# Performance work log

Hardware: AMD Instinct MI355X
Metric: run time of the kernel (lower is better)

## Reference

```python
import jax, jax.numpy as jnp
import numpy as np

B, L, D, H, NLAYERS = 32, 2048, 1024, 16, 4
HD = D // H
NEG = -1e30


def setup_inputs() -> dict:
    key = jax.random.key(0)
    ks = jax.random.split(key, 12)
    tokens = jax.random.normal(ks[0], (B, L, D), dtype=jnp.float32)
    lengths = jax.random.randint(ks[1], (B,), 1, L + 1, dtype=jnp.int32)
    query_token = jax.random.normal(ks[2], (1, D), dtype=jnp.float32)
    s = 0.02
    Wq = jax.random.normal(ks[3], (NLAYERS, D, D), dtype=jnp.float32) * s
    Wk = jax.random.normal(ks[4], (NLAYERS, D, D), dtype=jnp.float32) * s
    Wv = jax.random.normal(ks[5], (NLAYERS, D, D), dtype=jnp.float32) * s
    Wo = jax.random.normal(ks[6], (NLAYERS, D, D), dtype=jnp.float32) * s
    bq = jnp.zeros((NLAYERS, D), jnp.float32)
    bk = jnp.zeros((NLAYERS, D), jnp.float32)
    bv = jnp.zeros((NLAYERS, D), jnp.float32)
    bo = jnp.zeros((NLAYERS, D), jnp.float32)
    gamma = jnp.ones((NLAYERS, D), jnp.float32)
    beta = jnp.zeros((NLAYERS, D), jnp.float32)
    return dict(tokens=tokens, lengths=lengths, query_token=query_token,
                Wq=Wq, bq=bq, Wk=Wk, bk=bk, Wv=Wv, bv=bv, Wo=Wo, bo=bo,
                gamma=gamma, beta=beta)


def _layernorm(x, g, b):
    mu = jnp.mean(x, axis=-1, keepdims=True)
    var = jnp.mean(jnp.square(x - mu), axis=-1, keepdims=True)
    return (x - mu) * jax.lax.rsqrt(var + 1e-5) * g + b


def reference(tokens, lengths, query_token, Wq, bq, Wk, bk, Wv, bv, Wo, bo, gamma, beta):
    # valid[b, l] = True where token l exists (inverse of key_padding_mask)
    valid = jnp.arange(L)[None, :] < lengths[:, None]            # [B, L]
    scale = 1.0 / jnp.sqrt(jnp.float32(HD))
    # zero out padded positions like the torch padded buffer (math-neutral)
    toks = tokens * valid[:, :, None].astype(tokens.dtype)       # [B, L, D]
    q = jnp.broadcast_to(query_token[None], (B, 1, D))           # [B, 1, D]
    for i in range(NLAYERS):
        qh = (q @ Wq[i] + bq[i]).reshape(B, 1, H, HD)            # [B, 1, H, hd]
        kh = (toks @ Wk[i] + bk[i]).reshape(B, L, H, HD)         # [B, L, H, hd]
        vh = (toks @ Wv[i] + bv[i]).reshape(B, L, H, HD)
        scores = jnp.einsum('bqhd,bkhd->bhqk', qh, kh) * scale   # [B, H, 1, L]
        scores = jnp.where(valid[:, None, None, :], scores, NEG)
        attn = jax.nn.softmax(scores, axis=-1)
        out = jnp.einsum('bhqk,bkhd->bqhd', attn, vh).reshape(B, 1, D)
        out = out @ Wo[i] + bo[i]
        q = _layernorm(out, gamma[i], beta[i])
    return q[:, 0, :]                                            # [B, D]
```

## Files before the change

kernel.cpp:

```cpp
#include <hip/hip_runtime.h>
#include <hip/hip_bf16.h>
#include <cstdint>
#include <cstddef>

#define BB 32
#define LL 2048
#define DD 1024
#define HH 16
#define HDIM 64
#define NL 4
#define NCHUNK 8
#define CHUNK 256
#define NEGINF -1e30f

typedef __attribute__((ext_vector_type(8))) short bf16x8;
typedef __attribute__((ext_vector_type(4))) float f32x4;

__device__ __forceinline__ unsigned short f2b(float x) {
    union { float f; unsigned int u; } v; v.f = x;
    unsigned int r = (v.u + 0x7FFFu + ((v.u >> 16) & 1u)) >> 16;
    return (unsigned short)r;
}

template<int SRC, int KSP>
__global__ __launch_bounds__(256) void k_gemv(
        const float* __restrict__ Xg,
        const float* __restrict__ stats, const float* __restrict__ gamma,
        const float* __restrict__ beta,
        const float* __restrict__ parts_in, const float* __restrict__ bias_in,
        const float* __restrict__ ctx_p, const float* __restrict__ m_p,
        const float* __restrict__ s_p,
        const float* __restrict__ W, float* __restrict__ outp) {
    constexpr int KL = DD / KSP;
    int bid = blockIdx.x, tid = threadIdx.x;
    int ct = bid & 15, ks = bid >> 4;
    int e0 = ks * KL;
    __shared__ float Xs[BB][KL];
    __shared__ float wgtS[BB][NCHUNK];
    __shared__ float mgS[BB], SgS[BB];
    if (SRC == 3) {
        if (tid < BB) {
            int b = tid; float m = NEGINF;
            for (int c8 = 0; c8 < NCHUNK; ++c8)
                m = fmaxf(m, m_p[(b * NCHUNK + c8) * HH + ct]);
            float S = 0.f;
            for (int c8 = 0; c8 < NCHUNK; ++c8)
                S += s_p[(b * NCHUNK + c8) * HH + ct] *
                     __expf(m_p[(b * NCHUNK + c8) * HH + ct] - m);
            mgS[b] = m; SgS[b] = S;
        }
        __syncthreads();
        {
            int b = tid >> 3, c8 = tid & 7;
            wgtS[b][c8] = __expf(m_p[(b * NCHUNK + c8) * HH + ct] - mgS[b]) / SgS[b];
        }
        __syncthreads();
    }
    for (int j = 0; j < (BB * KL) / 256; ++j) {
        int i = tid + j * 256;
        int b = i / KL, k = i % KL;
        float x;
        if (SRC == 0) {
            x = Xg[e0 + k];
        } else if (SRC == 1) {
            float mu = stats[b * 2], rstd = stats[b * 2 + 1];
            x = (Xg[(size_t)b * DD + e0 + k] - mu) * rstd * gamma[e0 + k] + beta[e0 + k];
        } else if (SRC == 2) {
            x = bias_in[e0 + k];
#pragma unroll
            for (int j2 = 0; j2 < 32; ++j2)
                x += parts_in[((size_t)(j2 * BB) + b) * DD + e0 + k];
        } else {
            x = 0.f;
#pragma unroll
            for (int c8 = 0; c8 < NCHUNK; ++c8)
                x += wgtS[b][c8] *
                     ctx_p[(((size_t)(b * NCHUNK + c8)) * HH + ct) * DD + e0 + k];
        }
        Xs[b][k] = x;
    }
    __syncthreads();
    int col = tid & 63, bg = tid >> 6;
    int c = ct * 64 + col;
    float acc[8] = {0.f, 0.f, 0.f, 0.f, 0.f, 0.f, 0.f, 0.f};
    for (int k = 0; k < KL; k += 4) {
        float w0 = W[(size_t)(e0 + k) * DD + c];
        float w1 = W[(size_t)(e0 + k + 1) * DD + c];
        float w2 = W[(size_t)(e0 + k + 2) * DD + c];
        float w3 = W[(size_t)(e0 + k + 3) * DD + c];
#pragma unroll
        for (int bb = 0; bb < 8; ++bb) {
            const float4 xv = *(const float4*)&Xs[bg * 8 + bb][k];
            acc[bb] += xv.x * w0 + xv.y * w1 + xv.z * w2 + xv.w * w3;
        }
    }
#pragma unroll
    for (int bb = 0; bb < 8; ++bb)
        outp[((size_t)(ks * BB) + bg * 8 + bb) * DD + c] = acc[bb];
}

__global__ __launch_bounds__(1024) void k_stats(const float* __restrict__ parts,
        const float* __restrict__ bo, float* __restrict__ oraw,
        float* __restrict__ stats) {
    int b = blockIdx.x, c = threadIdx.x;
    float v = bo[c];
#pragma unroll
    for (int ks = 0; ks < 8; ++ks)
        v += parts[((size_t)(ks * BB) + b) * DD + c];
    oraw[(size_t)b * DD + c] = v;
    float s1 = v, s2 = v * v;
#pragma unroll
    for (int off = 32; off; off >>= 1) {
        s1 += __shfl_xor(s1, off);
        s2 += __shfl_xor(s2, off);
    }
    __shared__ float r1[16], r2[16];
    int w = c >> 6;
    if ((c & 63) == 0) { r1[w] = s1; r2[w] = s2; }
    __syncthreads();
    if (c == 0) {
        float a = 0.f, q = 0.f;
#pragma unroll
        for (int i = 0; i < 16; ++i) { a += r1[i]; q += r2[i]; }
        float mu = a / (float)DD, var = q / (float)DD - mu * mu;
        stats[b * 2] = mu;
        stats[b * 2 + 1] = rsqrtf(var + 1e-5f);
    }
}

__global__ __launch_bounds__(256) void k_final(const float* __restrict__ oraw,
        const float* __restrict__ stats, const float* __restrict__ gamma,
        const float* __restrict__ beta, float* __restrict__ outp) {
    int i = blockIdx.x * 256 + threadIdx.x;
    int b = i >> 10, c = i & (DD - 1);
    outp[i] = (oraw[i] - stats[b * 2]) * stats[b * 2 + 1] * gamma[c] + beta[c];
}

__global__ __launch_bounds__(256) void k_wk(const float* __restrict__ qp,
        const float* __restrict__ bq,
        const float* __restrict__ Wk, const float* __restrict__ bk,
        unsigned short* __restrict__ wk16, float* __restrict__ sb) {
    int h = blockIdx.x >> 4, et = blockIdx.x & 15;
    int tid = threadIdx.x;
    __shared__ float qs[BB][HDIM + 1];
    for (int i = tid; i < BB * HDIM; i += 256) {
        int bb = i >> 6, d = i & 63;
        float v = bq[h * HDIM + d];
#pragma unroll
        for (int ks = 0; ks < 8; ++ks)
            v += qp[((size_t)(ks * BB + bb)) * DD + h * HDIM + d];
        qs[bb][d] = v;
    }
    __syncthreads();
    int b = tid & 31, eo = tid >> 5;
    for (int k = 0; k < 8; ++k) {
        int e = et * 64 + eo * 8 + k;
        const float* wrow = Wk + (size_t)e * DD + h * HDIM;
        float acc = 0.f;
#pragma unroll
        for (int d = 0; d < HDIM; ++d) acc += qs[b][d] * wrow[d];
        wk16[((size_t)(b * HH + h)) * DD + e] = f2b(acc);
    }
    if (et == 0 && tid < BB) {
        float acc = 0.f;
#pragma unroll
        for (int d = 0; d < HDIM; ++d) acc += qs[tid][d] * bk[h * HDIM + d];
        sb[tid * HH + h] = acc;
    }
}

template<int MODE>
__global__ __launch_bounds__(1024) void k_attn(const float* __restrict__ toks,
        unsigned short* __restrict__ tcache,
        const int* __restrict__ lens, const unsigned short* __restrict__ wk16,
        const float* __restrict__ sb, float* __restrict__ ctx_p,
        float* __restrict__ m_p, float* __restrict__ s_p) {
    int b = blockIdx.x >> 3, chunk = blockIdx.x & 7;
    int tid = threadIdx.x, lane = tid & 63, w = tid >> 6;
    int len = lens[b];
    int base = chunk * CHUNK;
    int pidx = (b * NCHUNK + chunk) * HH;
    if (base >= len) {
        if (tid < HH) { m_p[pidx + tid] = NEGINF; s_p[pidx + tid] = 0.f; }
        return;
    }
    int nv = min(CHUNK, len - base);
    int ng = (nv + 31) >> 5;

    __shared__ __align__(16) unsigned short Tr[32][1032];
    __shared__ float Sred[16][HH][34];
    __shared__ unsigned short Pt[HH][40];
    __shared__ float sm_m[HH], sm_s[HH], sm_c[HH];

    if (tid < HH) { sm_m[tid] = NEGINF; sm_s[tid] = 0.f; }

    int hq = lane & 15, qg = lane >> 4;
    const unsigned short* wkb = wk16 + ((size_t)(b * HH + hq)) * DD + w * 64 + 8 * qg;
    bf16x8 afr0 = *(const bf16x8*)(wkb);
    bf16x8 afr1 = *(const bf16x8*)(wkb + 32);
    f32x4 zer = {0.f, 0.f, 0.f, 0.f};
    f32x4 ctxacc[4] = {zer, zer, zer, zer};
    float sbh = (tid < 512) ? sb[b * HH + (tid >> 5)] : 0.f;
    int st = tid >> 7;
    int se = (tid & 127) * 8;
    const size_t rowbase = (size_t)(b * LL + base);

    bf16x8 pc[4];
    float4 pa[4], pb[4];
    auto LOADG = [&](int g) {
        if (MODE == 2) {
            const unsigned short* s0p = tcache + (rowbase + g * 32) * DD + se;
#pragma unroll
            for (int p = 0; p < 4; ++p)
                pc[p] = *(const bf16x8*)(s0p + (size_t)(p * 8 + st) * DD);
        } else {
            const float* s0p = toks + (rowbase + g * 32) * DD + se;
#pragma unroll
            for (int p = 0; p < 4; ++p) {
                const float* sp = s0p + (size_t)(p * 8 + st) * DD;
                pa[p] = *(const float4*)sp;
                pb[p] = *(const float4*)(sp + 4);
            }
        }
    };
    LOADG(0);
    __syncthreads();

    for (int g = 0; g < ng; ++g) {
        int t0 = g * 32;
        if (MODE == 2) {
#pragma unroll
            for (int p = 0; p < 4; ++p)
                *(bf16x8*)&Tr[p * 8 + st][se] = pc[p];
        } else {
#pragma unroll
            for (int p = 0; p < 4; ++p) {
                bf16x8 v;
                v[0] = f2b(pa[p].x); v[1] = f2b(pa[p].y);
                v[2] = f2b(pa[p].z); v[3] = f2b(pa[p].w);
                v[4] = f2b(pb[p].x); v[5] = f2b(pb[p].y);
                v[6] = f2b(pb[p].z); v[7] = f2b(pb[p].w);
                *(bf16x8*)&Tr[p * 8 + st][se] = v;
                if (MODE == 1)
                    *(bf16x8*)(tcache + (rowbase + t0 + p * 8 + st) * DD + se) = v;
            }
        }
        if (g + 1 < ng) LOADG(g + 1);
        __syncthreads();
        f32x4 s0 = zer, s1 = zer;
        {
            int eb = w * 64 + 8 * qg;
            s0 = __builtin_amdgcn_mfma_f32_16x16x32_bf16(afr0, *(const bf16x8*)&Tr[hq][eb], s0, 0, 0, 0);
            s0 = __builtin_amdgcn_mfma_f32_16x16x32_bf16(afr1, *(const bf16x8*)&Tr[hq][eb + 32], s0, 0, 0, 0);
            s1 = __builtin_amdgcn_mfma_f32_16x16x32_bf16(afr0, *(const bf16x8*)&Tr[16 + hq][eb], s1, 0, 0, 0);
            s1 = __builtin_amdgcn_mfma_f32_16x16x32_bf16(afr1, *(const bf16x8*)&Tr[16 + hq][eb + 32], s1, 0, 0, 0);
        }
#pragma unroll
        for (int r = 0; r < 4; ++r) {
            Sred[w][qg * 4 + r][hq] = s0[r];
            Sred[w][qg * 4 + r][16 + hq] = s1[r];
        }
        __syncthreads();
        if (tid < 512) {
            int h = tid >> 5, t = tid & 31;
            float s = 0.f;
#pragma unroll
            for (int ww = 0; ww < 16; ++ww) s += Sred[ww][h][t];
            s = (s + sbh) * 0.125f;
            bool valid = (t0 + t) < nv;
            if (!valid) s = NEGINF;
            float tm = s;
#pragma unroll
            for (int off = 16; off; off >>= 1) tm = fmaxf(tm, __shfl_xor(tm, off, 32));
            float oldm = sm_m[h];
            float newm = fmaxf(oldm, tm);
            float pv = valid ? __expf(s - newm) : 0.f;
            float ps = pv;
#pragma unroll
            for (int off = 16; off; off >>= 1) ps += __shfl_xor(ps, off, 32);
            if (t == 0) {
                float corr = __expf(oldm - newm);
                sm_c[h] = corr;
                sm_m[h] = newm;
                sm_s[h] = sm_s[h] * corr + ps;
            }
            Pt[h][t] = f2b(pv);
        }
        __syncthreads();
        {
            float cr[4];
#pragma unroll
            for (int r = 0; r < 4; ++r) cr[r] = sm_c[qg * 4 + r];
            bf16x8 pafr;
            ushort4 pa0 = *(const ushort4*)&Pt[hq][8 * qg];
            ushort4 pa1 = *(const ushort4*)&Pt[hq][8 * qg + 4];
            pafr[0] = pa0.x; pafr[1] = pa0.y; pafr[2] = pa0.z; pafr[3] = pa0.w;
            pafr[4] = pa1.x; pafr[5] = pa1.y; pafr[6] = pa1.z; pafr[7] = pa1.w;
#pragma unroll
            for (int et = 0; et < 4; ++et) {
#pragma unroll
                for (int r = 0; r < 4; ++r) ctxacc[et][r] *= cr[r];
                bf16x8 bfr;
                int ec = w * 64 + et * 16 + hq;
#pragma unroll
                for (int i = 0; i < 8; ++i) bfr[i] = (short)Tr[8 * qg + i][ec];
                ctxacc[et] = __builtin_amdgcn_mfma_f32_16x16x32_bf16(pafr, bfr, ctxacc[et], 0, 0, 0);
            }
        }
        __syncthreads();
    }
    if (tid < HH) { m_p[pidx + tid] = sm_m[tid]; s_p[pidx + tid] = sm_s[tid]; }
#pragma unroll
    for (int et = 0; et < 4; ++et)
#pragma unroll
        for (int r = 0; r < 4; ++r) {
            int h = qg * 4 + r, e = w * 64 + et * 16 + hq;
            ctx_p[((size_t)pidx + h) * DD + e] = ctxacc[et][r];
        }
}

extern "C" void kernel_launch(void* const* d_in, const int* in_sizes, int n_in,
                              void* d_out, int out_size, void* d_ws, size_t ws_size,
                              hipStream_t stream) {
    const float* toks  = (const float*)d_in[0];
    const int*   lens  = (const int*)d_in[1];
    const float* qt    = (const float*)d_in[2];
    const float* Wq    = (const float*)d_in[3];
    const float* bq    = (const float*)d_in[4];
    const float* Wk    = (const float*)d_in[5];
    const float* bk    = (const float*)d_in[6];
    const float* Wv    = (const float*)d_in[7];
    const float* bv    = (const float*)d_in[8];
    const float* Wo    = (const float*)d_in[9];
    const float* bo    = (const float*)d_in[10];
    const float* gamma = (const float*)d_in[11];
    const float* beta  = (const float*)d_in[12];
    float* out = (float*)d_out;
    float* ws  = (float*)d_ws;

    float* ctx_p = ws;
    float* m_p   = ws + 4194304;
    float* s_p   = ws + 4198400;
    float* pvp   = ws + 4202496;
    float* op    = ws + 5251072;
    float* qp    = ws + 5513216;
    float* oraw  = ws + 5775360;
    float* stats = ws + 5808128;
    float* sbuf  = ws + 5808192;
    unsigned short* wk16 = (unsigned short*)(ws + 5808704);
    const size_t base_floats = 6070848;
    unsigned short* tcache = (unsigned short*)(ws + base_floats);
    const size_t need_cache = base_floats * 4 + (size_t)BB * LL * DD * 2;
    const bool use_cache = (ws_size >= need_cache);

    k_gemv<0, 8><<<128, 256, 0, stream>>>(qt, nullptr, nullptr, nullptr,
            nullptr, nullptr, nullptr, nullptr, nullptr, Wq, qp);
    k_wk<<<256, 256, 0, stream>>>(qp, bq, Wk, bk, wk16, sbuf);

    for (int i = 0; i < NL; ++i) {
        if (use_cache) {
            if (i == 0)
                k_attn<1><<<256, 1024, 0, stream>>>(toks, tcache, lens, wk16,
                        sbuf, ctx_p, m_p, s_p);
            else
                k_attn<2><<<256, 1024, 0, stream>>>(toks, tcache, lens, wk16,
                        sbuf, ctx_p, m_p, s_p);
        } else {
            k_attn<0><<<256, 1024, 0, stream>>>(toks, tcache, lens, wk16,
                    sbuf, ctx_p, m_p, s_p);
        }
        const float* Wv_i = Wv + (size_t)i * DD * DD;
        const float* Wo_i = Wo + (size_t)i * DD * DD;
        k_gemv<3, 32><<<512, 256, 0, stream>>>(nullptr, nullptr, nullptr, nullptr,
                nullptr, nullptr, ctx_p, m_p, s_p, Wv_i, pvp);
        k_gemv<2, 8><<<128, 256, 0, stream>>>(nullptr, nullptr, nullptr, nullptr,
                pvp, bv + i * DD, nullptr, nullptr, nullptr, Wo_i, op);
        k_stats<<<32, 1024, 0, stream>>>(op, bo + i * DD, oraw, stats);
        if (i == NL - 1) {
            k_final<<<128, 256, 0, stream>>>(oraw, stats, gamma + i * DD,
                    beta + i * DD, out);
        } else {
            k_gemv<1, 8><<<128, 256, 0, stream>>>(oraw, stats, gamma + i * DD,
                    beta + i * DD, nullptr, nullptr, nullptr, nullptr, nullptr,
                    Wq + (size_t)(i + 1) * DD * DD, qp);
            k_wk<<<256, 256, 0, stream>>>(qp, bq + (i + 1) * DD,
                    Wk + (size_t)(i + 1) * DD * DD, bk + (i + 1) * DD,
                    wk16, sbuf);
        }
    }
}
```

Before: 402.6 us.

## Store attention partials in bf16, unify GEMV split, fuse final layernorm, drop prefetch

Attention partial context outputs are now written as bf16 instead of fp32, which halves the traffic between the attention kernel and the Wv GEMV. All GEMVs now use a uniform 16-way K split with 256 blocks, and the downstream reductions are adjusted to match. The final layernorm is folded into the stats kernel, removing one launch. The register prefetch of the next token group in the attention kernel is removed in favour of a simpler load-then-compute loop. The bf16 partials add rounding error, and losing the prefetch may expose load latency.

```diff
diff --git a/kernel.cpp b/kernel.cpp
--- a/kernel.cpp
+++ b/kernel.cpp
@@ -12,6 +12,7 @@
 #define NCHUNK 8
 #define CHUNK 256
 #define NEGINF -1e30f
+#define PKS 16
 
 typedef __attribute__((ext_vector_type(8))) short bf16x8;
 typedef __attribute__((ext_vector_type(4))) float f32x4;
@@ -21,17 +22,21 @@
     unsigned int r = (v.u + 0x7FFFu + ((v.u >> 16) & 1u)) >> 16;
     return (unsigned short)r;
 }
-
-template<int SRC, int KSP>
+__device__ __forceinline__ float b2f(unsigned short u) {
+    union { unsigned int u; float f; } v; v.u = ((unsigned int)u) << 16;
+    return v.f;
+}
+
+template<int SRC>
 __global__ __launch_bounds__(256) void k_gemv(
         const float* __restrict__ Xg,
         const float* __restrict__ stats, const float* __restrict__ gamma,
         const float* __restrict__ beta,
         const float* __restrict__ parts_in, const float* __restrict__ bias_in,
-        const float* __restrict__ ctx_p, const float* __restrict__ m_p,
+        const unsigned short* __restrict__ ctx16, const float* __restrict__ m_p,
         const float* __restrict__ s_p,
         const float* __restrict__ W, float* __restrict__ outp) {
-    constexpr int KL = DD / KSP;
+    constexpr int KL = DD / PKS;
     int bid = blockIdx.x, tid = threadIdx.x;
     int ct = bid & 15, ks = bid >> 4;
     int e0 = ks * KL;
@@ -56,9 +61,10 @@
         }
         __syncthreads();
     }
-    for (int j = 0; j < (BB * KL) / 256; ++j) {
+#pragma unroll
+    for (int j = 0; j < 8; ++j) {
         int i = tid + j * 256;
-        int b = i / KL, k = i % KL;
+        int b = i >> 6, k = i & 63;
         float x;
         if (SRC == 0) {
             x = Xg[e0 + k];
@@ -68,14 +74,14 @@
         } else if (SRC == 2) {
             x = bias_in[e0 + k];
 #pragma unroll
-            for (int j2 = 0; j2 < 32; ++j2)
+            for (int j2 = 0; j2 < PKS; ++j2)
                 x += parts_in[((size_t)(j2 * BB) + b) * DD + e0 + k];
         } else {
             x = 0.f;
 #pragma unroll
             for (int c8 = 0; c8 < NCHUNK; ++c8)
                 x += wgtS[b][c8] *
-                     ctx_p[(((size_t)(b * NCHUNK + c8)) * HH + ct) * DD + e0 + k];
+                     b2f(ctx16[(((size_t)(b * NCHUNK + c8)) * HH + ct) * DD + e0 + k]);
         }
         Xs[b][k] = x;
     }
@@ -99,15 +105,17 @@
         outp[((size_t)(ks * BB) + bg * 8 + bb) * DD + c] = acc[bb];
 }
 
+template<int LAST>
 __global__ __launch_bounds__(1024) void k_stats(const float* __restrict__ parts,
-        const float* __restrict__ bo, float* __restrict__ oraw,
-        float* __restrict__ stats) {
+        const float* __restrict__ bo, const float* __restrict__ gamma,
+        const float* __restrict__ beta, float* __restrict__ oraw,
+        float* __restrict__ stats, float* __restrict__ outp) {
     int b = blockIdx.x, c = threadIdx.x;
     float v = bo[c];
 #pragma unroll
-    for (int ks = 0; ks < 8; ++ks)
+    for (int ks = 0; ks < PKS; ++ks)
         v += parts[((size_t)(ks * BB) + b) * DD + c];
-    oraw[(size_t)b * DD + c] = v;
+    if (!LAST) oraw[(size_t)b * DD + c] = v;
     float s1 = v, s2 = v * v;
 #pragma unroll
     for (int off = 32; off; off >>= 1) {
@@ -115,6 +123,7 @@
         s2 += __shfl_xor(s2, off);
     }
     __shared__ float r1[16], r2[16];
+    __shared__ float smu, srs;
     int w = c >> 6;
     if ((c & 63) == 0) { r1[w] = s1; r2[w] = s2; }
     __syncthreads();
@@ -123,17 +132,14 @@
 #pragma unroll
         for (int i = 0; i < 16; ++i) { a += r1[i]; q += r2[i]; }
         float mu = a / (float)DD, var = q / (float)DD - mu * mu;
+        float rs = rsqrtf(var + 1e-5f);
+        smu = mu; srs = rs;
         stats[b * 2] = mu;
-        stats[b * 2 + 1] = rsqrtf(var + 1e-5f);
-    }
-}
-
-__global__ __launch_bounds__(256) void k_final(const float* __restrict__ oraw,
-        const float* __restrict__ stats, const float* __restrict__ gamma,
-        const float* __restrict__ beta, float* __restrict__ outp) {
-    int i = blockIdx.x * 256 + threadIdx.x;
-    int b = i >> 10, c = i & (DD - 1);
-    outp[i] = (oraw[i] - stats[b * 2]) * stats[b * 2 + 1] * gamma[c] + beta[c];
+        stats[b * 2 + 1] = rs;
+    }
+    __syncthreads();
+    if (LAST)
+        outp[(size_t)b * DD + c] = (v - smu) * srs * gamma[c] + beta[c];
 }
 
 __global__ __launch_bounds__(256) void k_wk(const float* __restrict__ qp,
@@ -147,7 +153,7 @@
         int bb = i >> 6, d = i & 63;
         float v = bq[h * HDIM + d];
 #pragma unroll
-        for (int ks = 0; ks < 8; ++ks)
+        for (int ks = 0; ks < PKS; ++ks)
             v += qp[((size_t)(ks * BB + bb)) * DD + h * HDIM + d];
         qs[bb][d] = v;
     }
@@ -173,7 +179,7 @@
 __global__ __launch_bounds__(1024) void k_attn(const float* __restrict__ toks,
         unsigned short* __restrict__ tcache,
         const int* __restrict__ lens, const unsigned short* __restrict__ wk16,
-        const float* __restrict__ sb, float* __restrict__ ctx_p,
+        const float* __restrict__ sb, unsigned short* __restrict__ ctx16,
         float* __restrict__ m_p, float* __restrict__ s_p) {
     int b = blockIdx.x >> 3, chunk = blockIdx.x & 7;
     int tid = threadIdx.x, lane = tid & 63, w = tid >> 6;
@@ -185,7 +191,6 @@
         return;
     }
     int nv = min(CHUNK, len - base);
-    int ng = (nv + 31) >> 5;
 
     __shared__ __align__(16) unsigned short Tr[32][1032];
     __shared__ float Sred[16][HH][34];
@@ -203,49 +208,35 @@
     float sbh = (tid < 512) ? sb[b * HH + (tid >> 5)] : 0.f;
     int st = tid >> 7;
     int se = (tid & 127) * 8;
-    const size_t rowbase = (size_t)(b * LL + base);
-
-    bf16x8 pc[4];
-    float4 pa[4], pb[4];
-    auto LOADG = [&](int g) {
+    __syncthreads();
+
+    for (int g = 0; g < 8; ++g) {
+        int t0 = g * 32;
+        if (t0 >= nv) break;
         if (MODE == 2) {
-            const unsigned short* s0p = tcache + (rowbase + g * 32) * DD + se;
-#pragma unroll
-            for (int p = 0; p < 4; ++p)
-                pc[p] = *(const bf16x8*)(s0p + (size_t)(p * 8 + st) * DD);
+            const unsigned short* srcr = tcache + ((size_t)(b * LL + base + t0)) * DD;
+#pragma unroll
+            for (int p = 0; p < 4; ++p) {
+                int t = p * 8 + st;
+                bf16x8 v = *(const bf16x8*)(srcr + (size_t)t * DD + se);
+                *(bf16x8*)&Tr[t][se] = v;
+            }
         } else {
-            const float* s0p = toks + (rowbase + g * 32) * DD + se;
+            const float* srcr = toks + ((size_t)(b * LL + base + t0)) * DD;
 #pragma unroll
             for (int p = 0; p < 4; ++p) {
-                const float* sp = s0p + (size_t)(p * 8 + st) * DD;
-                pa[p] = *(const float4*)sp;
-                pb[p] = *(const float4*)(sp + 4);
+                int t = p * 8 + st;
+                const float* sp = srcr + (size_t)t * DD + se;
+                float4 a0 = *(const float4*)sp;
+                float4 a1 = *(const float4*)(sp + 4);
+                bf16x8 v;
+                v[0] = f2b(a0.x); v[1] = f2b(a0.y); v[2] = f2b(a0.z); v[3] = f2b(a0.w);
+                v[4] = f2b(a1.x); v[5] = f2b(a1.y); v[6] = f2b(a1.z); v[7] = f2b(a1.w);
+                *(bf16x8*)&Tr[t][se] = v;
+                if (MODE == 1)
+                    *(bf16x8*)(tcache + ((size_t)(b * LL + base + t0 + t)) * DD + se) = v;
             }
         }
-    };
-    LOADG(0);
-    __syncthreads();
-
-    for (int g = 0; g < ng; ++g) {
-        int t0 = g * 32;
-        if (MODE == 2) {
-#pragma unroll
-            for (int p = 0; p < 4; ++p)
-                *(bf16x8*)&Tr[p * 8 + st][se] = pc[p];
-        } else {
-#pragma unroll
-            for (int p = 0; p < 4; ++p) {
-                bf16x8 v;
-                v[0] = f2b(pa[p].x); v[1] = f2b(pa[p].y);
-                v[2] = f2b(pa[p].z); v[3] = f2b(pa[p].w);
-                v[4] = f2b(pb[p].x); v[5] = f2b(pb[p].y);
-                v[6] = f2b(pb[p].z); v[7] = f2b(pb[p].w);
-                *(bf16x8*)&Tr[p * 8 + st][se] = v;
-                if (MODE == 1)
-                    *(bf16x8*)(tcache + (rowbase + t0 + p * 8 + st) * DD + se) = v;
-            }
-        }
-        if (g + 1 < ng) LOADG(g + 1);
         __syncthreads();
         f32x4 s0 = zer, s1 = zer;
         {
@@ -315,7 +306,7 @@
 #pragma unroll
         for (int r = 0; r < 4; ++r) {
             int h = qg * 4 + r, e = w * 64 + et * 16 + hq;
-            ctx_p[((size_t)pidx + h) * DD + e] = ctxacc[et][r];
+            ctx16[((size_t)pidx + h) * DD + e] = f2b(ctxacc[et][r]);
         }
 }
 
@@ -338,22 +329,22 @@
     float* out = (float*)d_out;
     float* ws  = (float*)d_ws;
 
-    float* ctx_p = ws;
-    float* m_p   = ws + 4194304;
-    float* s_p   = ws + 4198400;
-    float* pvp   = ws + 4202496;
-    float* op    = ws + 5251072;
-    float* qp    = ws + 5513216;
-    float* oraw  = ws + 5775360;
-    float* stats = ws + 5808128;
-    float* sbuf  = ws + 5808192;
-    unsigned short* wk16 = (unsigned short*)(ws + 5808704);
-    const size_t base_floats = 6070848;
+    unsigned short* ctx16 = (unsigned short*)ws;
+    float* m_p   = ws + 2097152;
+    float* s_p   = ws + 2101248;
+    float* pvp   = ws + 2105344;
+    float* op    = ws + 2629632;
+    float* qp    = ws + 3153920;
+    float* oraw  = ws + 3678208;
+    float* stats = ws + 3710976;
+    float* sbuf  = ws + 3711040;
+    unsigned short* wk16 = (unsigned short*)(ws + 3711552);
+    const size_t base_floats = 3973696;
     unsigned short* tcache = (unsigned short*)(ws + base_floats);
     const size_t need_cache = base_floats * 4 + (size_t)BB * LL * DD * 2;
     const bool use_cache = (ws_size >= need_cache);
 
-    k_gemv<0, 8><<<128, 256, 0, stream>>>(qt, nullptr, nullptr, nullptr,
+    k_gemv<0><<<256, 256, 0, stream>>>(qt, nullptr, nullptr, nullptr,
             nullptr, nullptr, nullptr, nullptr, nullptr, Wq, qp);
     k_wk<<<256, 256, 0, stream>>>(qp, bq, Wk, bk, wk16, sbuf);
 
@@ -361,26 +352,27 @@
         if (use_cache) {
             if (i == 0)
                 k_attn<1><<<256, 1024, 0, stream>>>(toks, tcache, lens, wk16,
-                        sbuf, ctx_p, m_p, s_p);
+                        sbuf, ctx16, m_p, s_p);
             else
                 k_attn<2><<<256, 1024, 0, stream>>>(toks, tcache, lens, wk16,
-                        sbuf, ctx_p, m_p, s_p);
+                        sbuf, ctx16, m_p, s_p);
         } else {
             k_attn<0><<<256, 1024, 0, stream>>>(toks, tcache, lens, wk16,
-                    sbuf, ctx_p, m_p, s_p);
+                    sbuf, ctx16, m_p, s_p);
         }
         const float* Wv_i = Wv + (size_t)i * DD * DD;
         const float* Wo_i = Wo + (size_t)i * DD * DD;
-        k_gemv<3, 32><<<512, 256, 0, stream>>>(nullptr, nullptr, nullptr, nullptr,
-                nullptr, nullptr, ctx_p, m_p, s_p, Wv_i, pvp);
-        k_gemv<2, 8><<<128, 256, 0, stream>>>(nullptr, nullptr, nullptr, nullptr,
+        k_gemv<3><<<256, 256, 0, stream>>>(nullptr, nullptr, nullptr, nullptr,
+                nullptr, nullptr, ctx16, m_p, s_p, Wv_i, pvp);
+        k_gemv<2><<<256, 256, 0, stream>>>(nullptr, nullptr, nullptr, nullptr,
                 pvp, bv + i * DD, nullptr, nullptr, nullptr, Wo_i, op);
-        k_stats<<<32, 1024, 0, stream>>>(op, bo + i * DD, oraw, stats);
         if (i == NL - 1) {
-            k_final<<<128, 256, 0, stream>>>(oraw, stats, gamma + i * DD,
-                    beta + i * DD, out);
+            k_stats<1><<<32, 1024, 0, stream>>>(op, bo + i * DD, gamma + i * DD,
+                    beta + i * DD, oraw, stats, out);
         } else {
-            k_gemv<1, 8><<<128, 256, 0, stream>>>(oraw, stats, gamma + i * DD,
+            k_stats<0><<<32, 1024, 0, stream>>>(op, bo + i * DD, gamma + i * DD,
+                    beta + i * DD, oraw, stats, out);
+            k_gemv<1><<<256, 256, 0, stream>>>(oraw, stats, gamma + i * DD,
                     beta + i * DD, nullptr, nullptr, nullptr, nullptr, nullptr,
                     Wq + (size_t)(i + 1) * DD * DD, qp);
             k_wk<<<256, 256, 0, stream>>>(qp, bq + (i + 1) * DD,
```

New measurement: 353.9 us. -12.1%, faster.
